# Kernel tuning notes

Hardware: AMD Instinct MI355X
Metric: run time of the kernel (lower is better)

Reference implementation:

```python
import jax, jax.numpy as jnp
import numpy as np

B, C, H, W = 32, 512, 56, 56


def setup_inputs() -> dict:
    key = jax.random.key(0)
    k1, k2, k3 = jax.random.split(key, 3)
    x = jax.random.normal(k1, (B, C, H, W), dtype=jnp.float32)
    scale = 1.0 / np.sqrt(C)  # kaiming-ish init for bias-free Linear(C, C)
    W1 = jax.random.normal(k2, (C, C), dtype=jnp.float32) * scale  # fc (sigmoid gate)
    W3 = jax.random.normal(k3, (C, C), dtype=jnp.float32) * scale  # fc3 (relu gate)
    return {"x": x, "W1": W1, "W3": W3}


def reference(x, W1, W3):
    x = jax.nn.relu(x)
    # Stage 1: peak-vs-avg region suppression (per (b,c) spatial reductions)
    avg_region = jnp.mean(x, axis=(2, 3), keepdims=True)   # [B,C,1,1]
    peak_region = jnp.max(x, axis=(2, 3), keepdims=True)   # [B,C,1,1]
    x = jnp.where((peak_region - avg_region) < 0.5, 0.0, x)
    # Stage 2: channel max/mean exp-based gating
    cmax = jnp.max(x, axis=1, keepdims=True)               # [B,1,H,W]
    cmean = jnp.mean(x, axis=1, keepdims=True)             # [B,1,H,W]
    bb = 1.0 - jnp.exp(-jnp.abs(cmax - cmean))
    x = bb * x
    # Stage 3: max extractor
    x_max = jnp.max(x, axis=(2, 3), keepdims=True)         # [B,C,1,1]
    # Stages 4-5: suppression controllers (global avg pool -> FC gates)
    pooled = jnp.mean(x, axis=(2, 3))                      # [B,C]
    control1 = jax.nn.sigmoid(pooled @ W1.T)[:, :, None, None]
    control3 = jax.nn.relu(pooled @ W3.T)
    control3 = jnp.where(control3 < 1.0, 1.2, control3)[:, :, None, None]
    thres = control1 * control3 * x_max                    # [B,C,1,1]
    return jnp.where(x < thres, 0.0, x)
```

## Files before the change

### kernel.cpp

```cpp
#include <hip/hip_runtime.h>

#define NB 32
#define NC 512
#define NH 56
#define NW 56
#define HW 3136
#define CHW 1605632
#define CCH 64
#define LSTR 60

__global__ __launch_bounds__(256) void k1_mask(const float* __restrict__ x,
                                               float* __restrict__ mask) {
    const int plane = blockIdx.x;
    const float4* px = (const float4*)(x + (size_t)plane * HW);
    float lmax = 0.f;
    double lsum = 0.0;
    for (int i = threadIdx.x; i < HW / 4; i += 256) {
        float4 v = px[i];
        float f0 = fmaxf(v.x, 0.f), f1 = fmaxf(v.y, 0.f);
        float f2 = fmaxf(v.z, 0.f), f3 = fmaxf(v.w, 0.f);
        lmax = fmaxf(lmax, fmaxf(fmaxf(f0, f1), fmaxf(f2, f3)));
        lsum += (double)f0 + (double)f1 + (double)f2 + (double)f3;
    }
    for (int off = 32; off; off >>= 1) {
        lsum += __shfl_xor(lsum, off);
        lmax = fmaxf(lmax, __shfl_xor(lmax, off));
    }
    __shared__ double ssum[4];
    __shared__ float smax[4];
    int wid = threadIdx.x >> 6, lane = threadIdx.x & 63;
    if (lane == 0) { ssum[wid] = lsum; smax[wid] = lmax; }
    __syncthreads();
    if (threadIdx.x == 0) {
        double s = ssum[0] + ssum[1] + ssum[2] + ssum[3];
        float m = fmaxf(fmaxf(smax[0], smax[1]), fmaxf(smax[2], smax[3]));
        float avg = (float)(s / 3136.0);
        mask[plane] = ((m - avg) < 0.5f) ? 0.f : 1.f;
    }
}

__global__ __launch_bounds__(256) void k2a_bb(const float* __restrict__ x,
                                              const float* __restrict__ mask,
                                              float* __restrict__ bb) {
    const int bh = blockIdx.x;
    const int b = bh / NH, h = bh % NH;
    __shared__ float lds[CCH * LSTR];
    __shared__ float sm[4][NW];
    __shared__ double ss[4][NW];
    const int tid = threadIdx.x;
    const size_t base = (size_t)b * CHW + (size_t)h * NW;
    const int w = tid % NW, q = tid / NW;
    float cmax = 0.f;
    double csum = 0.0;
    for (int c0 = 0; c0 < NC; c0 += CCH) {
        for (int i = tid; i < CCH * 14; i += 256) {
            int cl = i / 14, w4 = (i % 14) * 4;
            float4 v = *(const float4*)(x + base + (size_t)(c0 + cl) * HW + w4);
            float mk = mask[b * NC + c0 + cl];
            v.x = fmaxf(v.x, 0.f) * mk;
            v.y = fmaxf(v.y, 0.f) * mk;
            v.z = fmaxf(v.z, 0.f) * mk;
            v.w = fmaxf(v.w, 0.f) * mk;
            *(float4*)(&lds[cl * LSTR + w4]) = v;
        }
        __syncthreads();
        if (tid < 224) {
#pragma unroll
            for (int i = 0; i < CCH / 4; i++) {
                float f = lds[(q + 4 * i) * LSTR + w];
                cmax = fmaxf(cmax, f);
                csum += (double)f;
            }
        }
        __syncthreads();
    }
    if (tid < 224) { sm[q][w] = cmax; ss[q][w] = csum; }
    __syncthreads();
    if (tid < NW) {
        float m = fmaxf(fmaxf(sm[0][tid], sm[1][tid]), fmaxf(sm[2][tid], sm[3][tid]));
        double s = ss[0][tid] + ss[1][tid] + ss[2][tid] + ss[3][tid];
        double cmean = s * (1.0 / 512.0);
        double d = fabs((double)m - cmean);
        bb[(size_t)b * HW + h * NW + tid] = (float)(1.0 - exp(-d));
    }
}

__global__ __launch_bounds__(256) void k2b_stats(const float* __restrict__ x,
                                                 const float* __restrict__ mask,
                                                 const float* __restrict__ bb,
                                                 float* __restrict__ xmax,
                                                 float* __restrict__ pooled) {
    const int plane = blockIdx.x;
    const int b = plane >> 9;
    const float4* px = (const float4*)(x + (size_t)plane * HW);
    const float4* pbb = (const float4*)(bb + (size_t)b * HW);
    const float mk = mask[plane];
    float m = 0.f;
    double s = 0.0;
    for (int i = threadIdx.x; i < HW / 4; i += 256) {
        float4 v = px[i];
        float4 bv = pbb[i];
        float x0 = fmaxf(v.x, 0.f) * mk * bv.x;
        float x1 = fmaxf(v.y, 0.f) * mk * bv.y;
        float x2 = fmaxf(v.z, 0.f) * mk * bv.z;
        float x3 = fmaxf(v.w, 0.f) * mk * bv.w;
        m = fmaxf(m, fmaxf(fmaxf(x0, x1), fmaxf(x2, x3)));
        s += (double)x0 + (double)x1 + (double)x2 + (double)x3;
    }
    for (int off = 32; off; off >>= 1) {
        s += __shfl_xor(s, off);
        m = fmaxf(m, __shfl_xor(m, off));
    }
    __shared__ double ssum[4];
    __shared__ float smax[4];
    int wid = threadIdx.x >> 6, lane = threadIdx.x & 63;
    if (lane == 0) { ssum[wid] = s; smax[wid] = m; }
    __syncthreads();
    if (threadIdx.x == 0) {
        double st = ssum[0] + ssum[1] + ssum[2] + ssum[3];
        float mt = fmaxf(fmaxf(smax[0], smax[1]), fmaxf(smax[2], smax[3]));
        xmax[plane] = mt;
        pooled[plane] = (float)(st / 3136.0);
    }
}

__global__ __launch_bounds__(256) void k3_gates(const float* __restrict__ pooled,
                                                const float* __restrict__ W1,
                                                const float* __restrict__ W3,
                                                const float* __restrict__ xmax,
                                                float* __restrict__ thres) {
    int wave = threadIdx.x >> 6, lane = threadIdx.x & 63;
    int task0 = (blockIdx.x * 4 + wave) * 4;
    for (int t = 0; t < 4; t++) {
        int task = task0 + t;
        int b = task >> 9, j = task & 511;
        const float* r1 = W1 + j * 512;
        const float* r3 = W3 + j * 512;
        const float* pr = pooled + b * 512;
        double s1 = 0.0, s3 = 0.0;
        for (int k = lane; k < 512; k += 64) {
            double p = (double)pr[k];
            s1 += p * (double)r1[k];
            s3 += p * (double)r3[k];
        }
        for (int off = 32; off; off >>= 1) {
            s1 += __shfl_xor(s1, off);
            s3 += __shfl_xor(s3, off);
        }
        if (lane == 0) {
            float c1 = (float)(1.0 / (1.0 + exp(-s1)));
            double r = s3 > 0.0 ? s3 : 0.0;
            float c3 = (float)((r < 1.0) ? 1.2 : r);
            thres[task] = c1 * c3 * xmax[task];
        }
    }
}

__global__ __launch_bounds__(256) void k4_out(const float* __restrict__ x,
                                              const float* __restrict__ mask,
                                              const float* __restrict__ bb,
                                              const float* __restrict__ thres,
                                              float* __restrict__ out) {
    const int plane = blockIdx.x;
    const int b = plane >> 9;
    const float4* px = (const float4*)(x + (size_t)plane * HW);
    float4* po = (float4*)(out + (size_t)plane * HW);
    const float4* pbb = (const float4*)(bb + (size_t)b * HW);
    const float th = thres[plane];
    const float mk = mask[plane];
    for (int i = threadIdx.x; i < HW / 4; i += 256) {
        float4 v = px[i];
        float4 bv = pbb[i];
        float x0 = fmaxf(v.x, 0.f) * mk * bv.x;
        float x1 = fmaxf(v.y, 0.f) * mk * bv.y;
        float x2 = fmaxf(v.z, 0.f) * mk * bv.z;
        float x3 = fmaxf(v.w, 0.f) * mk * bv.w;
        float4 o;
        o.x = (x0 < th) ? 0.f : x0;
        o.y = (x1 < th) ? 0.f : x1;
        o.z = (x2 < th) ? 0.f : x2;
        o.w = (x3 < th) ? 0.f : x3;
        po[i] = o;
    }
}

extern "C" void kernel_launch(void* const* d_in, const int* in_sizes, int n_in,
                              void* d_out, int out_size, void* d_ws, size_t ws_size,
                              hipStream_t stream) {
    const float* x  = (const float*)d_in[0];
    const float* W1 = (const float*)d_in[1];
    const float* W3 = (const float*)d_in[2];
    float* out = (float*)d_out;
    float* ws = (float*)d_ws;
    float* mask   = ws;
    float* bb     = ws + 16384;
    float* xmax   = ws + 116736;
    float* pooled = ws + 133120;
    float* thres  = ws + 149504;

    hipLaunchKernelGGL(k1_mask,    dim3(NB * NC), dim3(256), 0, stream, x, mask);
    hipLaunchKernelGGL(k2a_bb,     dim3(NB * NH), dim3(256), 0, stream, x, mask, bb);
    hipLaunchKernelGGL(k2b_stats,  dim3(NB * NC), dim3(256), 0, stream, x, mask, bb, xmax, pooled);
    hipLaunchKernelGGL(k3_gates,   dim3(1024),    dim3(256), 0, stream, pooled, W1, W3, xmax, thres);
    hipLaunchKernelGGL(k4_out,     dim3(NB * NC), dim3(256), 0, stream, x, mask, bb, thres, out);
}
```

Baseline: 465.6 us.

## Fuse channel-gate and per-plane stats into one tiled pass with atomics

Replaces the separate bb kernel and the stats kernel with one fused kernel. It loads a 512-channel by 32-pixel tile into LDS, computes the bb gate for those pixels, and then accumulates per-channel sums and maxes into global memory with double atomicAdd and integer atomicMax. This removes one full read of x, which is about 205 MB. In exchange it adds about 70 KB of LDS per block, which limits occupancy, plus many atomics on 16K addresses and two small init and finalize kernels. The atomic sum order also makes the result nondeterministic.

```diff
diff --git a/kernel.cpp b/kernel.cpp
--- a/kernel.cpp
+++ b/kernel.cpp
@@ -6,8 +6,8 @@
 #define NW 56
 #define HW 3136
 #define CHW 1605632
-#define CCH 64
-#define LSTR 60
+#define NT 98
+#define TP 32
 
 __global__ __launch_bounds__(256) void k1_mask(const float* __restrict__ x,
                                                float* __restrict__ mask) {
@@ -39,95 +39,93 @@
     }
 }
 
-__global__ __launch_bounds__(256) void k2a_bb(const float* __restrict__ x,
-                                              const float* __restrict__ mask,
-                                              float* __restrict__ bb) {
-    const int bh = blockIdx.x;
-    const int b = bh / NH, h = bh % NH;
-    __shared__ float lds[CCH * LSTR];
-    __shared__ float sm[4][NW];
-    __shared__ double ss[4][NW];
+__global__ __launch_bounds__(256) void k0_init(double* __restrict__ pooled64,
+                                               int* __restrict__ xmaxI) {
+    int i = blockIdx.x * 256 + threadIdx.x;
+    pooled64[i] = 0.0;
+    xmaxI[i] = 0;
+}
+
+__global__ __launch_bounds__(256) void k2_fused(const float* __restrict__ x,
+                                                const float* __restrict__ mask,
+                                                float* __restrict__ bb,
+                                                double* __restrict__ pooled64,
+                                                int* __restrict__ xmaxI) {
+    const int blk = blockIdx.x;
+    const int b = blk / NT, t = blk % NT;
+    extern __shared__ char smem[];
+    double* sums = (double*)smem;
+    float*  xs   = (float*)(smem + 2048);
+    float*  maxs = (float*)(smem + 2048 + 65536);
+    float*  bbv  = (float*)(smem + 2048 + 65536 + 1024);
+    float*  maskl= (float*)(smem + 2048 + 65536 + 1024 + 128);
     const int tid = threadIdx.x;
-    const size_t base = (size_t)b * CHW + (size_t)h * NW;
-    const int w = tid % NW, q = tid / NW;
-    float cmax = 0.f;
-    double csum = 0.0;
-    for (int c0 = 0; c0 < NC; c0 += CCH) {
-        for (int i = tid; i < CCH * 14; i += 256) {
-            int cl = i / 14, w4 = (i % 14) * 4;
-            float4 v = *(const float4*)(x + base + (size_t)(c0 + cl) * HW + w4);
-            float mk = mask[b * NC + c0 + cl];
-            v.x = fmaxf(v.x, 0.f) * mk;
-            v.y = fmaxf(v.y, 0.f) * mk;
-            v.z = fmaxf(v.z, 0.f) * mk;
-            v.w = fmaxf(v.w, 0.f) * mk;
-            *(float4*)(&lds[cl * LSTR + w4]) = v;
-        }
-        __syncthreads();
-        if (tid < 224) {
-#pragma unroll
-            for (int i = 0; i < CCH / 4; i++) {
-                float f = lds[(q + 4 * i) * LSTR + w];
-                cmax = fmaxf(cmax, f);
-                csum += (double)f;
-            }
-        }
-        __syncthreads();
-    }
-    if (tid < 224) { sm[q][w] = cmax; ss[q][w] = csum; }
-    __syncthreads();
-    if (tid < NW) {
-        float m = fmaxf(fmaxf(sm[0][tid], sm[1][tid]), fmaxf(sm[2][tid], sm[3][tid]));
-        double s = ss[0][tid] + ss[1][tid] + ss[2][tid] + ss[3][tid];
+    maskl[tid]       = mask[b * NC + tid];
+    maskl[tid + 256] = mask[b * NC + tid + 256];
+    __syncthreads();
+    const size_t base = (size_t)b * CHW + t * TP;
+    for (int i = tid; i < NC * 8; i += 256) {
+        int cl = i >> 3, v4 = (i & 7) * 4;
+        float4 v = *(const float4*)(x + base + (size_t)cl * HW + v4);
+        float mk = maskl[cl];
+        v.x = fmaxf(v.x, 0.f) * mk;
+        v.y = fmaxf(v.y, 0.f) * mk;
+        v.z = fmaxf(v.z, 0.f) * mk;
+        v.w = fmaxf(v.w, 0.f) * mk;
+        *(float4*)(&xs[cl * TP + v4]) = v;
+    }
+    __syncthreads();
+    {
+        int p = tid & 31, q = tid >> 5;
+        float cmax = 0.f;
+        double csum = 0.0;
+        for (int i = 0; i < NC / 8; i++) {
+            float f = xs[(q + 8 * i) * TP + p];
+            cmax = fmaxf(cmax, f);
+            csum += (double)f;
+        }
+        sums[q * 32 + p] = csum;
+        maxs[q * 32 + p] = cmax;
+    }
+    __syncthreads();
+    if (tid < TP) {
+        double s = 0.0;
+        float m = 0.f;
+        for (int q = 0; q < 8; q++) { s += sums[q * 32 + tid]; m = fmaxf(m, maxs[q * 32 + tid]); }
         double cmean = s * (1.0 / 512.0);
         double d = fabs((double)m - cmean);
-        bb[(size_t)b * HW + h * NW + tid] = (float)(1.0 - exp(-d));
-    }
-}
-
-__global__ __launch_bounds__(256) void k2b_stats(const float* __restrict__ x,
-                                                 const float* __restrict__ mask,
-                                                 const float* __restrict__ bb,
-                                                 float* __restrict__ xmax,
-                                                 float* __restrict__ pooled) {
-    const int plane = blockIdx.x;
-    const int b = plane >> 9;
-    const float4* px = (const float4*)(x + (size_t)plane * HW);
-    const float4* pbb = (const float4*)(bb + (size_t)b * HW);
-    const float mk = mask[plane];
-    float m = 0.f;
-    double s = 0.0;
-    for (int i = threadIdx.x; i < HW / 4; i += 256) {
-        float4 v = px[i];
-        float4 bv = pbb[i];
-        float x0 = fmaxf(v.x, 0.f) * mk * bv.x;
-        float x1 = fmaxf(v.y, 0.f) * mk * bv.y;
-        float x2 = fmaxf(v.z, 0.f) * mk * bv.z;
-        float x3 = fmaxf(v.w, 0.f) * mk * bv.w;
-        m = fmaxf(m, fmaxf(fmaxf(x0, x1), fmaxf(x2, x3)));
-        s += (double)x0 + (double)x1 + (double)x2 + (double)x3;
-    }
-    for (int off = 32; off; off >>= 1) {
-        s += __shfl_xor(s, off);
-        m = fmaxf(m, __shfl_xor(m, off));
-    }
-    __shared__ double ssum[4];
-    __shared__ float smax[4];
-    int wid = threadIdx.x >> 6, lane = threadIdx.x & 63;
-    if (lane == 0) { ssum[wid] = s; smax[wid] = m; }
-    __syncthreads();
-    if (threadIdx.x == 0) {
-        double st = ssum[0] + ssum[1] + ssum[2] + ssum[3];
-        float mt = fmaxf(fmaxf(smax[0], smax[1]), fmaxf(smax[2], smax[3]));
-        xmax[plane] = mt;
-        pooled[plane] = (float)(st / 3136.0);
-    }
+        float bv = (float)(1.0 - exp(-d));
+        bbv[tid] = bv;
+        bb[(size_t)b * HW + t * TP + tid] = bv;
+    }
+    __syncthreads();
+    for (int cc = 0; cc < 2; cc++) {
+        int c = tid + cc * 256;
+        const float* row = &xs[c * TP];
+        float m = 0.f;
+        double s = 0.0;
+#pragma unroll
+        for (int j = 0; j < TP; j++) {
+            int p = (j + tid) & 31;
+            float v = row[p] * bbv[p];
+            m = fmaxf(m, v);
+            s += (double)v;
+        }
+        atomicAdd(&pooled64[b * NC + c], s);
+        atomicMax(&xmaxI[b * NC + c], __float_as_int(m));
+    }
+}
+
+__global__ __launch_bounds__(256) void k2f_final(const double* __restrict__ pooled64,
+                                                 float* __restrict__ pooledF) {
+    int i = blockIdx.x * 256 + threadIdx.x;
+    pooledF[i] = (float)(pooled64[i] / 3136.0);
 }
 
 __global__ __launch_bounds__(256) void k3_gates(const float* __restrict__ pooled,
                                                 const float* __restrict__ W1,
                                                 const float* __restrict__ W3,
-                                                const float* __restrict__ xmax,
+                                                const float* __restrict__ xmaxF,
                                                 float* __restrict__ thres) {
     int wave = threadIdx.x >> 6, lane = threadIdx.x & 63;
     int task0 = (blockIdx.x * 4 + wave) * 4;
@@ -151,7 +149,7 @@
             float c1 = (float)(1.0 / (1.0 + exp(-s1)));
             double r = s3 > 0.0 ? s3 : 0.0;
             float c3 = (float)((r < 1.0) ? 1.2 : r);
-            thres[task] = c1 * c3 * xmax[task];
+            thres[task] = c1 * c3 * xmaxF[task];
         }
     }
 }
@@ -191,16 +189,23 @@
     const float* W1 = (const float*)d_in[1];
     const float* W3 = (const float*)d_in[2];
     float* out = (float*)d_out;
-    float* ws = (float*)d_ws;
-    float* mask   = ws;
-    float* bb     = ws + 16384;
-    float* xmax   = ws + 116736;
-    float* pooled = ws + 133120;
-    float* thres  = ws + 149504;
-
-    hipLaunchKernelGGL(k1_mask,    dim3(NB * NC), dim3(256), 0, stream, x, mask);
-    hipLaunchKernelGGL(k2a_bb,     dim3(NB * NH), dim3(256), 0, stream, x, mask, bb);
-    hipLaunchKernelGGL(k2b_stats,  dim3(NB * NC), dim3(256), 0, stream, x, mask, bb, xmax, pooled);
-    hipLaunchKernelGGL(k3_gates,   dim3(1024),    dim3(256), 0, stream, pooled, W1, W3, xmax, thres);
-    hipLaunchKernelGGL(k4_out,     dim3(NB * NC), dim3(256), 0, stream, x, mask, bb, thres, out);
-}
+    char* ws = (char*)d_ws;
+    double* pooled64 = (double*)ws;
+    int*    xmaxI    = (int*)(ws + 131072);
+    float*  mask     = (float*)(ws + 196608);
+    float*  bb       = (float*)(ws + 262144);
+    float*  pooledF  = (float*)(ws + 663552);
+    float*  thres    = (float*)(ws + 729088);
+
+    (void)hipFuncSetAttribute((const void*)k2_fused,
+                              hipFuncAttributeMaxDynamicSharedMemorySize, 70784);
+
+    hipLaunchKernelGGL(k1_mask,  dim3(NB * NC), dim3(256), 0, stream, x, mask);
+    hipLaunchKernelGGL(k0_init,  dim3(64),      dim3(256), 0, stream, pooled64, xmaxI);
+    hipLaunchKernelGGL(k2_fused, dim3(NB * NT), dim3(256), 70784, stream,
+                       x, mask, bb, pooled64, xmaxI);
+    hipLaunchKernelGGL(k2f_final, dim3(64),     dim3(256), 0, stream, pooled64, pooledF);
+    hipLaunchKernelGGL(k3_gates, dim3(1024),    dim3(256), 0, stream,
+                       pooledF, W1, W3, (const float*)xmaxI, thres);
+    hipLaunchKernelGGL(k4_out,   dim3(NB * NC), dim3(256), 0, stream, x, mask, bb, thres, out);
+}
```

New measurement: 466.3 us. No clear change (+0.1%).
